# Performance work log

Measured on AMD Instinct MI355X. Metric: run time of the kernel, lower is better.

Reference implementation:

```python
import jax, jax.numpy as jnp
import numpy as np

B, S, D = 8, 1024, 768
H, DH = 8, 96          # number_of_heads, head_outdim = D // H
DFF = 4 * D            # mlp hidden
EPS = 1e-5


def _p(key, shape, scale=0.02):
    return (jax.random.normal(key, shape, dtype=jnp.float32) * scale)


def setup_inputs() -> dict:
    key = jax.random.key(0)
    ks = jax.random.split(key, 16)
    return {
        "h": jax.random.normal(ks[0], (B, S, D), dtype=jnp.float32),
        "x": jax.random.normal(ks[1], (B, S, D), dtype=jnp.float32),
        # SLN 1: scalar gamma/beta + LayerNorm affine
        "g1": jnp.ones((), jnp.float32), "be1": jnp.zeros((), jnp.float32),
        "ln1_w": jnp.ones((D,), jnp.float32), "ln1_b": jnp.zeros((D,), jnp.float32),
        # SLN 2
        "g2": jnp.ones((), jnp.float32), "be2": jnp.zeros((), jnp.float32),
        "ln2_w": jnp.ones((D,), jnp.float32), "ln2_b": jnp.zeros((D,), jnp.float32),
        # MSA projections (stored as [in, out] for x @ W)
        "Wq": _p(ks[2], (D, H * DH)), "bq": jnp.zeros((H * DH,), jnp.float32),
        "Wk": _p(ks[3], (D, H * DH)), "bk": jnp.zeros((H * DH,), jnp.float32),
        "Wv": _p(ks[4], (D, H * DH)), "bv": jnp.zeros((H * DH,), jnp.float32),
        "Wo": _p(ks[5], (H * DH, D)), "bo": jnp.zeros((D,), jnp.float32),
        # MLP: D -> 4D -> D, relu
        "W1": _p(ks[6], (D, DFF)), "b1": jnp.zeros((DFF,), jnp.float32),
        "W2": _p(ks[7], (DFF, D)), "b2": jnp.zeros((D,), jnp.float32),
    }


def _sln(h, x, gamma, beta, w, b):
    # SLN(h, x) = gamma * x * LayerNorm(h) + beta * x
    mu = jnp.mean(h, axis=-1, keepdims=True)
    var = jnp.var(h, axis=-1, keepdims=True)
    ln = (h - mu) * jax.lax.rsqrt(var + EPS) * w + b
    return gamma * x * ln + beta * x


def _l2_msa(h, Wq, bq, Wk, bk, Wv, bv, Wo, bo):
    # L2-distance multi-head self-attention (lp=2)
    def heads(W, bias):
        y = h @ W + bias                      # [B,S,H*DH]
        return y.reshape(B, S, H, DH).transpose(0, 2, 1, 3)  # [B,H,S,DH]
    q, k, v = heads(Wq, bq), heads(Wk, bk), heads(Wv, bv)
    # pairwise L2 distances via the quadratic expansion (avoids [B,H,S,S,DH])
    q2 = jnp.sum(q * q, axis=-1)              # [B,H,S]
    k2 = jnp.sum(k * k, axis=-1)              # [B,H,S]
    qk = jnp.einsum("bhsd,bhtd->bhst", q, k)  # [B,H,S,S]
    d2 = jnp.maximum(q2[..., :, None] + k2[..., None, :] - 2.0 * qk, 0.0)
    dist = jnp.sqrt(d2)                       # cdist(q, k, p=2)
    attn = jax.nn.softmax(-dist / np.sqrt(DH), axis=-1)
    out = jnp.einsum("bhst,bhtd->bhsd", attn, v)  # [B,H,S,DH]
    out = out.transpose(0, 2, 1, 3).reshape(B, S, H * DH)
    return out @ Wo + bo


def reference(h, x, g1, be1, ln1_w, ln1_b, g2, be2, ln2_w, ln2_b,
              Wq, bq, Wk, bk, Wv, bv, Wo, bo, W1, b1, W2, b2):
    h1 = _sln(h, x, g1, be1, ln1_w, ln1_b)
    htmp = _l2_msa(h1, Wq, bq, Wk, bk, Wv, bv, Wo, bo) + h   # dropout_rate=0 -> identity
    h2 = _sln(htmp, x, g2, be2, ln2_w, ln2_b)
    hf = jax.nn.relu(h2 @ W1 + b1) @ W2 + b2 + htmp
    return (x, hf)
```

## Files before the change

kernel.cpp:

```cpp
#include <hip/hip_runtime.h>
#include <math.h>

#define B_ 8
#define S_ 1024
#define D_ 768
#define H_ 8
#define DH_ 96
#define DFF_ 3072
#define NTOK (B_*S_)
#define QKVW 2304
#define EPS_ 1e-5f

typedef __attribute__((ext_vector_type(4))) float f4;
typedef __attribute__((ext_vector_type(4))) int i4;
typedef __attribute__((ext_vector_type(8))) __bf16 bf16x8;
typedef __attribute__((ext_vector_type(4))) unsigned short us4;
typedef __attribute__((ext_vector_type(8))) unsigned short us8;

static __device__ __forceinline__ unsigned short f2bf(float f) {
    unsigned int u = __builtin_bit_cast(unsigned int, f);
    u += 0x7fffu + ((u >> 16) & 1u);
    return (unsigned short)(u >> 16);
}
static __device__ __forceinline__ float bf2f(unsigned short u) {
    unsigned int x = ((unsigned int)u) << 16;
    return __builtin_bit_cast(float, x);
}

#define GLOBAL_LOAD_LDS16(g, l) \
    __builtin_amdgcn_global_load_lds((const __attribute__((address_space(1))) unsigned int*)(g), \
                                     (__attribute__((address_space(3))) unsigned int*)(l), 16, 0, 0)

__global__ __launch_bounds__(192) void sln_kernel(
    const float* __restrict__ h, const float* __restrict__ x,
    const float* __restrict__ gamma, const float* __restrict__ beta,
    const float* __restrict__ w, const float* __restrict__ bvec,
    unsigned short* __restrict__ out_bf, float* __restrict__ xcopy)
{
    int row = blockIdx.x;
    int t = threadIdx.x;
    const float4* h4 = (const float4*)(h + (size_t)row * D_);
    const float4* x4 = (const float4*)(x + (size_t)row * D_);
    float4 hv = h4[t];
    float s  = hv.x + hv.y + hv.z + hv.w;
    float ss = hv.x*hv.x + hv.y*hv.y + hv.z*hv.z + hv.w*hv.w;
    #pragma unroll
    for (int off = 32; off > 0; off >>= 1) {
        s  += __shfl_down(s, off);
        ss += __shfl_down(ss, off);
    }
    __shared__ float red[2][3];
    int wid = t >> 6;
    if ((t & 63) == 0) { red[0][wid] = s; red[1][wid] = ss; }
    __syncthreads();
    float sum   = red[0][0] + red[0][1] + red[0][2];
    float sumsq = red[1][0] + red[1][1] + red[1][2];
    float mu  = sum * (1.0f / D_);
    float var = sumsq * (1.0f / D_) - mu * mu;
    float rstd = rsqrtf(var + EPS_);
    float g = gamma[0], be = beta[0];
    float4 wv = ((const float4*)w)[t];
    float4 bv = ((const float4*)bvec)[t];
    float4 xv = x4[t];
    us4 o;
    o.x = f2bf(xv.x * (g * ((hv.x - mu) * rstd * wv.x + bv.x) + be));
    o.y = f2bf(xv.y * (g * ((hv.y - mu) * rstd * wv.y + bv.y) + be));
    o.z = f2bf(xv.z * (g * ((hv.z - mu) * rstd * wv.z + bv.z) + be));
    o.w = f2bf(xv.w * (g * ((hv.w - mu) * rstd * wv.w + bv.w) + be));
    *(us4*)(out_bf + (size_t)row * D_ + t * 4) = o;
    if (xcopy) ((float4*)(xcopy + (size_t)row * D_))[t] = xv;
}

__global__ __launch_bounds__(256) void transpose_bf16_kernel(
    const float* __restrict__ in, unsigned short* __restrict__ out, int K, int N)
{
    __shared__ float tile[32][33];
    int n0 = blockIdx.x * 32, k0 = blockIdx.y * 32;
    int tx = threadIdx.x, ty = threadIdx.y;
    #pragma unroll
    for (int r = 0; r < 4; r++)
        tile[ty + r * 8][tx] = in[(size_t)(k0 + ty + r * 8) * N + n0 + tx];
    __syncthreads();
    #pragma unroll
    for (int r = 0; r < 4; r++)
        out[(size_t)(n0 + ty + r * 8) * K + k0 + tx] = f2bf(tile[tx][ty + r * 8]);
}

__global__ void concat_bias_kernel(const float* __restrict__ bq, const float* __restrict__ bk,
                                   const float* __restrict__ bv, float* __restrict__ outb)
{
    int i = blockIdx.x * 256 + threadIdx.x;
    if (i >= QKVW) return;
    float v = (i < 768) ? bq[i] : (i < 1536) ? bk[i - 768] : bv[i - 1536];
    outb[i] = v;
}

template<int OUT_BF16, int RELU>
__global__ __launch_bounds__(256) void gemm_mfma_kernel(
    const unsigned short* __restrict__ A, const unsigned short* __restrict__ Bt,
    const float* __restrict__ bias, const float* __restrict__ resid,
    void* __restrict__ Cout, int M, int N, int K)
{
    __shared__ unsigned short Asm[128 * 32];
    __shared__ unsigned short Bsm[128 * 32];

    int t = threadIdx.x;
    int lane = t & 63, wv = t >> 6;
    int wm = wv & 1, wn = wv >> 1;
    int l16 = lane & 15, quad = lane >> 4;

    int bm = blockIdx.x * 128;
    int bn = blockIdx.y * 128;

    const unsigned short* Abase = A  + (size_t)bm * K;
    const unsigned short* Bbase = Bt + (size_t)bn * K;

    int fl0 = t, fl1 = 256 + t;
    int r0s = fl0 >> 2, kc0 = (fl0 & 3) << 3;
    int r1s = fl1 >> 2, kc1 = (fl1 & 3) << 3;

    f4 acc[4][4] = {};

    for (int k0 = 0; k0 < K; k0 += 32) {
        __syncthreads();
        GLOBAL_LOAD_LDS16(Abase + (size_t)r0s * K + k0 + kc0, &Asm[fl0 * 8]);
        GLOBAL_LOAD_LDS16(Abase + (size_t)r1s * K + k0 + kc1, &Asm[fl1 * 8]);
        GLOBAL_LOAD_LDS16(Bbase + (size_t)r0s * K + k0 + kc0, &Bsm[fl0 * 8]);
        GLOBAL_LOAD_LDS16(Bbase + (size_t)r1s * K + k0 + kc1, &Bsm[fl1 * 8]);
        __syncthreads();

        bf16x8 xf[4], wf[4];
        #pragma unroll
        for (int i = 0; i < 4; i++) {
            int m = wm * 64 + i * 16 + l16;
            xf[i] = __builtin_bit_cast(bf16x8, *(const i4*)&Asm[m * 32 + quad * 8]);
        }
        #pragma unroll
        for (int j = 0; j < 4; j++) {
            int n = wn * 64 + j * 16 + l16;
            wf[j] = __builtin_bit_cast(bf16x8, *(const i4*)&Bsm[n * 32 + quad * 8]);
        }
        #pragma unroll
        for (int j = 0; j < 4; j++)
            #pragma unroll
            for (int i = 0; i < 4; i++)
                acc[j][i] = __builtin_amdgcn_mfma_f32_16x16x32_bf16(wf[j], xf[i], acc[j][i], 0, 0, 0);
    }

    #pragma unroll
    for (int i = 0; i < 4; i++) {
        int rowg = bm + wm * 64 + i * 16 + l16;
        #pragma unroll
        for (int j = 0; j < 4; j++) {
            int colg0 = bn + wn * 64 + j * 16 + quad * 4;
            f4 v = acc[j][i];
            f4 b4 = *(const f4*)&bias[colg0];
            v += b4;
            if (RELU) {
                #pragma unroll
                for (int r = 0; r < 4; r++) v[r] = fmaxf(v[r], 0.f);
            }
            if (resid) {
                f4 r4 = *(const f4*)&resid[(size_t)rowg * N + colg0];
                v += r4;
            }
            if (OUT_BF16) {
                us4 o;
                o.x = f2bf(v[0]); o.y = f2bf(v[1]); o.z = f2bf(v[2]); o.w = f2bf(v[3]);
                *(us4*)((unsigned short*)Cout + (size_t)rowg * N + colg0) = o;
            } else {
                *(f4*)((float*)Cout + (size_t)rowg * N + colg0) = v;
            }
        }
    }
}

__global__ __launch_bounds__(256) void norms_kernel(
    const unsigned short* __restrict__ qkv, float* __restrict__ q2g, float* __restrict__ k2g)
{
    int row = blockIdx.x;
    int t = threadIdx.x;
    int hh = t >> 5, l32 = t & 31;
    const unsigned short* base = qkv + (size_t)row * QKVW + hh * DH_ + l32 * 3;
    float qs = 0.f, ks = 0.f;
    #pragma unroll
    for (int e = 0; e < 3; e++) {
        float qv = bf2f(base[e]);
        float kv = bf2f(base[768 + e]);
        qs += qv * qv; ks += kv * kv;
    }
    #pragma unroll
    for (int off = 16; off > 0; off >>= 1) {
        qs += __shfl_xor(qs, off, 32);
        ks += __shfl_xor(ks, off, 32);
    }
    if (l32 == 0) {
        int b = row >> 10, s = row & 1023;
        int idx = (b * H_ + hh) * S_ + s;
        q2g[idx] = qs; k2g[idx] = ks;
    }
}

__global__ __launch_bounds__(256) void vtrans_kernel(
    const unsigned short* __restrict__ qkv, unsigned short* __restrict__ vt)
{
    __shared__ unsigned short Vl[64][100];
    int blk = blockIdx.x;
    int bh = blk >> 4, kt = blk & 15;
    int b = bh >> 3, hh = bh & 7;
    int t = threadIdx.x;
    int key = t >> 2, qc = t & 3;
    const unsigned short* src = qkv + ((size_t)(b * S_ + kt * 64 + key)) * QKVW + 1536 + hh * DH_;
    #pragma unroll
    for (int i = 0; i < 3; i++) {
        int chunk = qc + i * 4;
        us8 v = *(const us8*)(src + chunk * 8);
        #pragma unroll
        for (int e = 0; e < 8; e++) Vl[key][chunk * 8 + e] = v[e];
    }
    __syncthreads();
    unsigned short* dst = vt + (size_t)blk * 7168;
    #pragma unroll
    for (int r = 0; r < 3; r++) {
        int c = r * 256 + t;
        int vd = c >> 3, kc = c & 7;
        us8 o;
        #pragma unroll
        for (int j = 0; j < 8; j++) o[j] = Vl[kc * 8 + j][vd];
        *(us8*)(dst + vd * 72 + kc * 8) = o;
    }
}

__global__ __launch_bounds__(256, 2) void attn_mfma_kernel(
    const unsigned short* __restrict__ qkv,
    const unsigned short* __restrict__ vt,
    const float* __restrict__ q2g, const float* __restrict__ k2g,
    unsigned short* __restrict__ outb)
{
    __shared__ unsigned short Klds[64 * 96];
    __shared__ unsigned short Vlds[7168];
    __shared__ unsigned short Plds[4][32 * 72];

    int t = threadIdx.x;
    int lane = t & 63, w = t >> 6;
    int l16 = lane & 15, quad = lane >> 4;

    int bh = blockIdx.x >> 3;
    int qt = blockIdx.x & 7;
    int b = bh >> 3, hh = bh & 7;

    int qrow0 = qt * 128 + w * 32;

    const unsigned short* qb = qkv + ((size_t)(b * S_ + qrow0)) * QKVW + hh * DH_;
    bf16x8 qf[2][3];
    #pragma unroll
    for (int n = 0; n < 2; n++)
        #pragma unroll
        for (int d = 0; d < 3; d++)
            qf[n][d] = __builtin_bit_cast(bf16x8,
                *(const i4*)(qb + (size_t)(n * 16 + l16) * QKVW + d * 32 + quad * 8));

    float q2n[2];
    q2n[0] = q2g[bh * S_ + qrow0 + l16];
    q2n[1] = q2g[bh * S_ + qrow0 + 16 + l16];

    float mrun[2] = {-INFINITY, -INFINITY};
    float lrun[2] = {0.f, 0.f};
    f4 Oacc[2][6] = {};

    const float rs = 0.10206207261596575f;

    const unsigned short* kgb = qkv + ((size_t)(b * S_)) * QKVW + 768 + hh * DH_;
    const unsigned short* vgb0 = vt + (size_t)(bh * 16) * 7168;

    for (int it = 0; it < 16; it++) {
        __syncthreads();
        #pragma unroll
        for (int r = 0; r < 3; r++) {
            int c = r * 256 + t;
            int key = c / 12, dc = c % 12;
            GLOBAL_LOAD_LDS16(kgb + ((size_t)(it * 64 + key)) * QKVW + dc * 8, &Klds[c * 8]);
        }
        const unsigned short* vgb = vgb0 + (size_t)it * 7168;
        #pragma unroll
        for (int r = 0; r < 3; r++)
            GLOBAL_LOAD_LDS16(vgb + (r * 256 + t) * 8, &Vlds[(r * 256 + t) * 8]);
        if (t < 128)
            GLOBAL_LOAD_LDS16(vgb + (768 + t) * 8, &Vlds[(768 + t) * 8]);
        __syncthreads();

        f4 sf[4][2];
        #pragma unroll
        for (int kt2 = 0; kt2 < 4; kt2++) {
            bf16x8 kf[3];
            #pragma unroll
            for (int d = 0; d < 3; d++)
                kf[d] = __builtin_bit_cast(bf16x8,
                    *(const i4*)&Klds[(kt2 * 16 + l16) * 96 + d * 32 + quad * 8]);
            #pragma unroll
            for (int n = 0; n < 2; n++) {
                f4 a = {};
                #pragma unroll
                for (int d = 0; d < 3; d++)
                    a = __builtin_amdgcn_mfma_f32_16x16x32_bf16(kf[d], qf[n][d], a, 0, 0, 0);
                sf[kt2][n] = a;
            }
        }
        #pragma unroll
        for (int kt2 = 0; kt2 < 4; kt2++) {
            float4 k2f = *(const float4*)(k2g + bh * S_ + it * 64 + kt2 * 16 + quad * 4);
            float k2a[4] = {k2f.x, k2f.y, k2f.z, k2f.w};
            #pragma unroll
            for (int n = 0; n < 2; n++) {
                f4 s = sf[kt2][n];
                #pragma unroll
                for (int r2 = 0; r2 < 4; r2++) {
                    float d2 = fmaxf(q2n[n] + k2a[r2] - 2.f * s[r2], 0.f);
                    s[r2] = -sqrtf(d2) * rs;
                }
                sf[kt2][n] = s;
            }
        }
        float alph[2];
        #pragma unroll
        for (int n = 0; n < 2; n++) {
            f4 m4 = sf[0][n];
            #pragma unroll
            for (int kt2 = 1; kt2 < 4; kt2++)
                #pragma unroll
                for (int r2 = 0; r2 < 4; r2++)
                    m4[r2] = fmaxf(m4[r2], sf[kt2][n][r2]);
            float mx = fmaxf(fmaxf(m4[0], m4[1]), fmaxf(m4[2], m4[3]));
            mx = fmaxf(mx, __shfl_xor(mx, 16, 64));
            mx = fmaxf(mx, __shfl_xor(mx, 32, 64));
            float mnew = fmaxf(mrun[n], mx);
            alph[n] = __expf(mrun[n] - mnew);
            mrun[n] = mnew;
            float ssum = 0.f;
            #pragma unroll
            for (int kt2 = 0; kt2 < 4; kt2++) {
                f4 s = sf[kt2][n];
                #pragma unroll
                for (int r2 = 0; r2 < 4; r2++) { s[r2] = __expf(s[r2] - mnew); ssum += s[r2]; }
                sf[kt2][n] = s;
            }
            ssum += __shfl_xor(ssum, 16, 64);
            ssum += __shfl_xor(ssum, 32, 64);
            lrun[n] = lrun[n] * alph[n] + ssum;
            #pragma unroll
            for (int kt2 = 0; kt2 < 4; kt2++) {
                f4 s = sf[kt2][n];
                uint2 pk;
                pk.x = (unsigned)f2bf(s[0]) | ((unsigned)f2bf(s[1]) << 16);
                pk.y = (unsigned)f2bf(s[2]) | ((unsigned)f2bf(s[3]) << 16);
                *(uint2*)&Plds[w][(n * 16 + l16) * 72 + kt2 * 16 + quad * 4] = pk;
            }
        }
        f4 av0, av1;
        #pragma unroll
        for (int r2 = 0; r2 < 4; r2++) {
            int src = quad * 4 + r2;
            av0[r2] = __shfl(alph[0], src, 64);
            av1[r2] = __shfl(alph[1], src, 64);
        }
        #pragma unroll
        for (int vtl = 0; vtl < 6; vtl++)
            #pragma unroll
            for (int r2 = 0; r2 < 4; r2++) {
                Oacc[0][vtl][r2] *= av0[r2];
                Oacc[1][vtl][r2] *= av1[r2];
            }
        bf16x8 pa[2][2];
        #pragma unroll
        for (int mt = 0; mt < 2; mt++)
            #pragma unroll
            for (int kf2 = 0; kf2 < 2; kf2++)
                pa[mt][kf2] = __builtin_bit_cast(bf16x8,
                    *(const i4*)&Plds[w][(mt * 16 + l16) * 72 + kf2 * 32 + quad * 8]);
        #pragma unroll
        for (int vtl = 0; vtl < 6; vtl++) {
            bf16x8 vf0 = __builtin_bit_cast(bf16x8,
                *(const i4*)&Vlds[(vtl * 16 + l16) * 72 + quad * 8]);
            bf16x8 vf1 = __builtin_bit_cast(bf16x8,
                *(const i4*)&Vlds[(vtl * 16 + l16) * 72 + 32 + quad * 8]);
            #pragma unroll
            for (int mt = 0; mt < 2; mt++) {
                Oacc[mt][vtl] = __builtin_amdgcn_mfma_f32_16x16x32_bf16(pa[mt][0], vf0, Oacc[mt][vtl], 0, 0, 0);
                Oacc[mt][vtl] = __builtin_amdgcn_mfma_f32_16x16x32_bf16(pa[mt][1], vf1, Oacc[mt][vtl], 0, 0, 0);
            }
        }
    }
    float inv0 = 1.f / lrun[0], inv1 = 1.f / lrun[1];
    f4 iv0, iv1;
    #pragma unroll
    for (int r2 = 0; r2 < 4; r2++) {
        int src = quad * 4 + r2;
        iv0[r2] = __shfl(inv0, src, 64);
        iv1[r2] = __shfl(inv1, src, 64);
    }
    #pragma unroll
    for (int mt = 0; mt < 2; mt++)
        #pragma unroll
        for (int vtl = 0; vtl < 6; vtl++)
            #pragma unroll
            for (int r2 = 0; r2 < 4; r2++) {
                int row = b * S_ + qrow0 + mt * 16 + quad * 4 + r2;
                float v = Oacc[mt][vtl][r2] * (mt == 0 ? iv0[r2] : iv1[r2]);
                outb[(size_t)row * D_ + hh * DH_ + vtl * 16 + l16] = f2bf(v);
            }
}

extern "C" void kernel_launch(void* const* d_in, const int* in_sizes, int n_in,
                              void* d_out, int out_size, void* d_ws, size_t ws_size,
                              hipStream_t stream)
{
    const float* h    = (const float*)d_in[0];
    const float* x    = (const float*)d_in[1];
    const float* g1   = (const float*)d_in[2];
    const float* be1  = (const float*)d_in[3];
    const float* ln1w = (const float*)d_in[4];
    const float* ln1b = (const float*)d_in[5];
    const float* g2   = (const float*)d_in[6];
    const float* be2  = (const float*)d_in[7];
    const float* ln2w = (const float*)d_in[8];
    const float* ln2b = (const float*)d_in[9];
    const float* Wq   = (const float*)d_in[10];
    const float* bq   = (const float*)d_in[11];
    const float* Wk   = (const float*)d_in[12];
    const float* bk   = (const float*)d_in[13];
    const float* Wv   = (const float*)d_in[14];
    const float* bv   = (const float*)d_in[15];
    const float* Wo   = (const float*)d_in[16];
    const float* bo   = (const float*)d_in[17];
    const float* W1   = (const float*)d_in[18];
    const float* b1   = (const float*)d_in[19];
    const float* W2   = (const float*)d_in[20];
    const float* b2   = (const float*)d_in[21];

    float* out = (float*)d_out;
    char* wsb = (char*)d_ws;
    const size_t ND = (size_t)NTOK * D_;

    size_t off = 0;
    unsigned short* W1t = (unsigned short*)(wsb + off); off += 4718592;
    unsigned short* W2t = (unsigned short*)(wsb + off); off += 4718592;
    float* bqkv = (float*)(wsb + off);                  off += 16384;
    float* htmp = (float*)(wsb + off);                  off += ND * 4;
    float* q2g  = (float*)(wsb + off);                  off += (size_t)B_ * H_ * S_ * 4;
    float* k2g  = (float*)(wsb + off);                  off += (size_t)B_ * H_ * S_ * 4;
    unsigned short* h2b = (unsigned short*)(wsb + off); off += ND * 2;
    size_t pool0 = off;
    unsigned short* Wqkvt = (unsigned short*)(wsb + off); off += 3538944;
    unsigned short* Wot   = (unsigned short*)(wsb + off); off += 1179648;
    unsigned short* h1b   = (unsigned short*)(wsb + off); off += ND * 2;
    unsigned short* vtg   = (unsigned short*)(wsb + off); off += (size_t)1024 * 14336;
    unsigned short* qkvb  = (unsigned short*)(wsb + off); off += (size_t)NTOK * QKVW * 2;
    unsigned short* attnb   = h1b;
    unsigned short* hiddenb = (unsigned short*)(wsb + pool0);

    dim3 tb(32, 8);
    transpose_bf16_kernel<<<dim3(768/32, 768/32), tb, 0, stream>>>(Wq, Wqkvt,              768, 768);
    transpose_bf16_kernel<<<dim3(768/32, 768/32), tb, 0, stream>>>(Wk, Wqkvt + 768*768,    768, 768);
    transpose_bf16_kernel<<<dim3(768/32, 768/32), tb, 0, stream>>>(Wv, Wqkvt + 2*768*768,  768, 768);
    transpose_bf16_kernel<<<dim3(768/32, 768/32), tb, 0, stream>>>(Wo, Wot, 768, 768);
    transpose_bf16_kernel<<<dim3(3072/32, 768/32), tb, 0, stream>>>(W1, W1t, 768, 3072);
    transpose_bf16_kernel<<<dim3(768/32, 3072/32), tb, 0, stream>>>(W2, W2t, 3072, 768);
    concat_bias_kernel<<<9, 256, 0, stream>>>(bq, bk, bv, bqkv);

    sln_kernel<<<NTOK, 192, 0, stream>>>(h, x, g1, be1, ln1w, ln1b, h1b, out);

    gemm_mfma_kernel<1, 0><<<dim3(NTOK/128, QKVW/128), 256, 0, stream>>>(
        h1b, Wqkvt, bqkv, nullptr, qkvb, NTOK, QKVW, D_);

    norms_kernel<<<NTOK, 256, 0, stream>>>(qkvb, q2g, k2g);
    vtrans_kernel<<<1024, 256, 0, stream>>>(qkvb, vtg);

    attn_mfma_kernel<<<512, 256, 0, stream>>>(qkvb, vtg, q2g, k2g, attnb);

    gemm_mfma_kernel<0, 0><<<dim3(NTOK/128, D_/128), 256, 0, stream>>>(
        attnb, Wot, bo, h, htmp, NTOK, D_, D_);

    sln_kernel<<<NTOK, 192, 0, stream>>>(htmp, x, g2, be2, ln2w, ln2b, h2b, nullptr);

    gemm_mfma_kernel<1, 1><<<dim3(NTOK/128, DFF_/128), 256, 0, stream>>>(
        h2b, W1t, b1, nullptr, hiddenb, NTOK, DFF_, D_);
    gemm_mfma_kernel<0, 0><<<dim3(NTOK/128, D_/128), 256, 0, stream>>>(
        hiddenb, W2t, b2, htmp, out + ND, NTOK, D_, DFF_);

    (void)in_sizes; (void)n_in; (void)out_size; (void)ws_size;
}
```

Baseline: 501.3 us.

## Halve attention query tile per wave and add 128x64 GEMM for N=768 outputs

The attention kernel now processes 16 query rows per wave instead of 32, doubling the grid to 1024 blocks. It raises the launch-bounds occupancy hint to 4 and switches softmax to exp2 with a folded scale constant. A new 128x64-tile GEMM kernel is used for the two projections with N=768, doubling their block count to improve CU fill. The trade-off is that each K/V tile loaded into LDS is reused by fewer query rows, so global and LDS traffic per useful FLOP rises.

Measured after the change: 468.7 us. 1.07x faster.

```diff
diff --git a/kernel.cpp b/kernel.cpp
--- a/kernel.cpp
+++ b/kernel.cpp
@@ -175,6 +175,85 @@
     }
 }
 
+template<int OUT_BF16, int RELU>
+__global__ __launch_bounds__(256) void gemm_mfma_n64_kernel(
+    const unsigned short* __restrict__ A, const unsigned short* __restrict__ Bt,
+    const float* __restrict__ bias, const float* __restrict__ resid,
+    void* __restrict__ Cout, int M, int N, int K)
+{
+    __shared__ unsigned short Asm[128 * 32];
+    __shared__ unsigned short Bsm[64 * 32];
+
+    int t = threadIdx.x;
+    int lane = t & 63, wv = t >> 6;
+    int wm = wv & 1, wn = wv >> 1;
+    int l16 = lane & 15, quad = lane >> 4;
+
+    int bm = blockIdx.x * 128;
+    int bn = blockIdx.y * 64;
+
+    const unsigned short* Abase = A  + (size_t)bm * K;
+    const unsigned short* Bbase = Bt + (size_t)bn * K;
+
+    int fl0 = t, fl1 = 256 + t;
+    int r0s = fl0 >> 2, kc0 = (fl0 & 3) << 3;
+    int r1s = fl1 >> 2, kc1 = (fl1 & 3) << 3;
+
+    f4 acc[2][4] = {};
+
+    for (int k0 = 0; k0 < K; k0 += 32) {
+        __syncthreads();
+        GLOBAL_LOAD_LDS16(Abase + (size_t)r0s * K + k0 + kc0, &Asm[fl0 * 8]);
+        GLOBAL_LOAD_LDS16(Abase + (size_t)r1s * K + k0 + kc1, &Asm[fl1 * 8]);
+        GLOBAL_LOAD_LDS16(Bbase + (size_t)r0s * K + k0 + kc0, &Bsm[fl0 * 8]);
+        __syncthreads();
+
+        bf16x8 xf[4], wf[2];
+        #pragma unroll
+        for (int i = 0; i < 4; i++) {
+            int m = wm * 64 + i * 16 + l16;
+            xf[i] = __builtin_bit_cast(bf16x8, *(const i4*)&Asm[m * 32 + quad * 8]);
+        }
+        #pragma unroll
+        for (int j = 0; j < 2; j++) {
+            int n = wn * 32 + j * 16 + l16;
+            wf[j] = __builtin_bit_cast(bf16x8, *(const i4*)&Bsm[n * 32 + quad * 8]);
+        }
+        #pragma unroll
+        for (int j = 0; j < 2; j++)
+            #pragma unroll
+            for (int i = 0; i < 4; i++)
+                acc[j][i] = __builtin_amdgcn_mfma_f32_16x16x32_bf16(wf[j], xf[i], acc[j][i], 0, 0, 0);
+    }
+
+    #pragma unroll
+    for (int i = 0; i < 4; i++) {
+        int rowg = bm + wm * 64 + i * 16 + l16;
+        #pragma unroll
+        for (int j = 0; j < 2; j++) {
+            int colg0 = bn + wn * 32 + j * 16 + quad * 4;
+            f4 v = acc[j][i];
+            f4 b4 = *(const f4*)&bias[colg0];
+            v += b4;
+            if (RELU) {
+                #pragma unroll
+                for (int r = 0; r < 4; r++) v[r] = fmaxf(v[r], 0.f);
+            }
+            if (resid) {
+                f4 r4 = *(const f4*)&resid[(size_t)rowg * N + colg0];
+                v += r4;
+            }
+            if (OUT_BF16) {
+                us4 o;
+                o.x = f2bf(v[0]); o.y = f2bf(v[1]); o.z = f2bf(v[2]); o.w = f2bf(v[3]);
+                *(us4*)((unsigned short*)Cout + (size_t)rowg * N + colg0) = o;
+            } else {
+                *(f4*)((float*)Cout + (size_t)rowg * N + colg0) = v;
+            }
+        }
+    }
+}
+
 __global__ __launch_bounds__(256) void norms_kernel(
     const unsigned short* __restrict__ qkv, float* __restrict__ q2g, float* __restrict__ k2g)
 {
@@ -231,7 +310,7 @@
     }
 }
 
-__global__ __launch_bounds__(256, 2) void attn_mfma_kernel(
+__global__ __launch_bounds__(256, 4) void attn_mfma_kernel(
     const unsigned short* __restrict__ qkv,
     const unsigned short* __restrict__ vt,
     const float* __restrict__ q2g, const float* __restrict__ k2g,
@@ -239,36 +318,32 @@
 {
     __shared__ unsigned short Klds[64 * 96];
     __shared__ unsigned short Vlds[7168];
-    __shared__ unsigned short Plds[4][32 * 72];
+    __shared__ unsigned short Plds[4][16 * 72];
 
     int t = threadIdx.x;
     int lane = t & 63, w = t >> 6;
     int l16 = lane & 15, quad = lane >> 4;
 
-    int bh = blockIdx.x >> 3;
-    int qt = blockIdx.x & 7;
+    int bh = blockIdx.x >> 4;
+    int qt = blockIdx.x & 15;
     int b = bh >> 3, hh = bh & 7;
 
-    int qrow0 = qt * 128 + w * 32;
+    int qrow0 = qt * 64 + w * 16;
 
     const unsigned short* qb = qkv + ((size_t)(b * S_ + qrow0)) * QKVW + hh * DH_;
-    bf16x8 qf[2][3];
-    #pragma unroll
-    for (int n = 0; n < 2; n++)
-        #pragma unroll
-        for (int d = 0; d < 3; d++)
-            qf[n][d] = __builtin_bit_cast(bf16x8,
-                *(const i4*)(qb + (size_t)(n * 16 + l16) * QKVW + d * 32 + quad * 8));
-
-    float q2n[2];
-    q2n[0] = q2g[bh * S_ + qrow0 + l16];
-    q2n[1] = q2g[bh * S_ + qrow0 + 16 + l16];
-
-    float mrun[2] = {-INFINITY, -INFINITY};
-    float lrun[2] = {0.f, 0.f};
-    f4 Oacc[2][6] = {};
-
-    const float rs = 0.10206207261596575f;
+    bf16x8 qf[3];
+    #pragma unroll
+    for (int d = 0; d < 3; d++)
+        qf[d] = __builtin_bit_cast(bf16x8,
+            *(const i4*)(qb + (size_t)l16 * QKVW + d * 32 + quad * 8));
+
+    float q2n = q2g[bh * S_ + qrow0 + l16];
+
+    float mrun = -INFINITY;
+    float lrun = 0.f;
+    f4 Oacc[6] = {};
+
+    const float cexp = 0.14724445f;
 
     const unsigned short* kgb = qkv + ((size_t)(b * S_)) * QKVW + 768 + hh * DH_;
     const unsigned short* vgb0 = vt + (size_t)(bh * 16) * 7168;
@@ -289,125 +364,92 @@
             GLOBAL_LOAD_LDS16(vgb + (768 + t) * 8, &Vlds[(768 + t) * 8]);
         __syncthreads();
 
-        f4 sf[4][2];
+        f4 sf[4];
         #pragma unroll
         for (int kt2 = 0; kt2 < 4; kt2++) {
-            bf16x8 kf[3];
-            #pragma unroll
-            for (int d = 0; d < 3; d++)
-                kf[d] = __builtin_bit_cast(bf16x8,
-                    *(const i4*)&Klds[(kt2 * 16 + l16) * 96 + d * 32 + quad * 8]);
-            #pragma unroll
-            for (int n = 0; n < 2; n++) {
-                f4 a = {};
-                #pragma unroll
-                for (int d = 0; d < 3; d++)
-                    a = __builtin_amdgcn_mfma_f32_16x16x32_bf16(kf[d], qf[n][d], a, 0, 0, 0);
-                sf[kt2][n] = a;
-            }
+            bf16x8 kf0 = __builtin_bit_cast(bf16x8, *(const i4*)&Klds[(kt2 * 16 + l16) * 96 + quad * 8]);
+            bf16x8 kf1 = __builtin_bit_cast(bf16x8, *(const i4*)&Klds[(kt2 * 16 + l16) * 96 + 32 + quad * 8]);
+            bf16x8 kf2 = __builtin_bit_cast(bf16x8, *(const i4*)&Klds[(kt2 * 16 + l16) * 96 + 64 + quad * 8]);
+            f4 a = {};
+            a = __builtin_amdgcn_mfma_f32_16x16x32_bf16(kf0, qf[0], a, 0, 0, 0);
+            a = __builtin_amdgcn_mfma_f32_16x16x32_bf16(kf1, qf[1], a, 0, 0, 0);
+            a = __builtin_amdgcn_mfma_f32_16x16x32_bf16(kf2, qf[2], a, 0, 0, 0);
+            sf[kt2] = a;
         }
         #pragma unroll
         for (int kt2 = 0; kt2 < 4; kt2++) {
             float4 k2f = *(const float4*)(k2g + bh * S_ + it * 64 + kt2 * 16 + quad * 4);
             float k2a[4] = {k2f.x, k2f.y, k2f.z, k2f.w};
+            f4 s = sf[kt2];
             #pragma unroll
-            for (int n = 0; n < 2; n++) {
-                f4 s = sf[kt2][n];
-                #pragma unroll
-                for (int r2 = 0; r2 < 4; r2++) {
-                    float d2 = fmaxf(q2n[n] + k2a[r2] - 2.f * s[r2], 0.f);
-                    s[r2] = -sqrtf(d2) * rs;
-                }
-                sf[kt2][n] = s;
-            }
-        }
-        float alph[2];
-        #pragma unroll
-        for (int n = 0; n < 2; n++) {
-            f4 m4 = sf[0][n];
+            for (int r2 = 0; r2 < 4; r2++) {
+                float d2 = fmaxf(q2n + k2a[r2] - 2.f * s[r2], 0.f);
+                s[r2] = -__builtin_amdgcn_sqrtf(d2) * cexp;
+            }
+            sf[kt2] = s;
+        }
+        f4 m4 = sf[0];
+        #pragma unroll
+        for (int kt2 = 1; kt2 < 4; kt2++)
             #pragma unroll
-            for (int kt2 = 1; kt2 < 4; kt2++)
-                #pragma unroll
-                for (int r2 = 0; r2 < 4; r2++)
-                    m4[r2] = fmaxf(m4[r2], sf[kt2][n][r2]);
-            float mx = fmaxf(fmaxf(m4[0], m4[1]), fmaxf(m4[2], m4[3]));
-            mx = fmaxf(mx, __shfl_xor(mx, 16, 64));
-            mx = fmaxf(mx, __shfl_xor(mx, 32, 64));
-            float mnew = fmaxf(mrun[n], mx);
-            alph[n] = __expf(mrun[n] - mnew);
-            mrun[n] = mnew;
-            float ssum = 0.f;
+            for (int r2 = 0; r2 < 4; r2++)
+                m4[r2] = fmaxf(m4[r2], sf[kt2][r2]);
+        float mx = fmaxf(fmaxf(m4[0], m4[1]), fmaxf(m4[2], m4[3]));
+        mx = fmaxf(mx, __shfl_xor(mx, 16, 64));
+        mx = fmaxf(mx, __shfl_xor(mx, 32, 64));
+        float mnew = fmaxf(mrun, mx);
+        float alph = exp2f(mrun - mnew);
+        mrun = mnew;
+        float ssum = 0.f;
+        #pragma unroll
+        for (int kt2 = 0; kt2 < 4; kt2++) {
+            f4 s = sf[kt2];
             #pragma unroll
-            for (int kt2 = 0; kt2 < 4; kt2++) {
-                f4 s = sf[kt2][n];
-                #pragma unroll
-                for (int r2 = 0; r2 < 4; r2++) { s[r2] = __expf(s[r2] - mnew); ssum += s[r2]; }
-                sf[kt2][n] = s;
-            }
-            ssum += __shfl_xor(ssum, 16, 64);
-            ssum += __shfl_xor(ssum, 32, 64);
-            lrun[n] = lrun[n] * alph[n] + ssum;
-            #pragma unroll
-            for (int kt2 = 0; kt2 < 4; kt2++) {
-                f4 s = sf[kt2][n];
-                uint2 pk;
-                pk.x = (unsigned)f2bf(s[0]) | ((unsigned)f2bf(s[1]) << 16);
-                pk.y = (unsigned)f2bf(s[2]) | ((unsigned)f2bf(s[3]) << 16);
-                *(uint2*)&Plds[w][(n * 16 + l16) * 72 + kt2 * 16 + quad * 4] = pk;
-            }
-        }
-        f4 av0, av1;
-        #pragma unroll
-        for (int r2 = 0; r2 < 4; r2++) {
-            int src = quad * 4 + r2;
-            av0[r2] = __shfl(alph[0], src, 64);
-            av1[r2] = __shfl(alph[1], src, 64);
-        }
+            for (int r2 = 0; r2 < 4; r2++) { s[r2] = exp2f(s[r2] - mnew); ssum += s[r2]; }
+            sf[kt2] = s;
+        }
+        ssum += __shfl_xor(ssum, 16, 64);
+        ssum += __shfl_xor(ssum, 32, 64);
+        lrun = lrun * alph + ssum;
+        #pragma unroll
+        for (int kt2 = 0; kt2 < 4; kt2++) {
+            f4 s = sf[kt2];
+            uint2 pk;
+            pk.x = (unsigned)f2bf(s[0]) | ((unsigned)f2bf(s[1]) << 16);
+            pk.y = (unsigned)f2bf(s[2]) | ((unsigned)f2bf(s[3]) << 16);
+            *(uint2*)&Plds[w][l16 * 72 + kt2 * 16 + quad * 4] = pk;
+        }
+        f4 av;
+        #pragma unroll
+        for (int r2 = 0; r2 < 4; r2++)
+            av[r2] = __shfl(alph, quad * 4 + r2, 64);
         #pragma unroll
         for (int vtl = 0; vtl < 6; vtl++)
             #pragma unroll
-            for (int r2 = 0; r2 < 4; r2++) {
-                Oacc[0][vtl][r2] *= av0[r2];
-                Oacc[1][vtl][r2] *= av1[r2];
-            }
-        bf16x8 pa[2][2];
-        #pragma unroll
-        for (int mt = 0; mt < 2; mt++)
-            #pragma unroll
-            for (int kf2 = 0; kf2 < 2; kf2++)
-                pa[mt][kf2] = __builtin_bit_cast(bf16x8,
-                    *(const i4*)&Plds[w][(mt * 16 + l16) * 72 + kf2 * 32 + quad * 8]);
+            for (int r2 = 0; r2 < 4; r2++)
+                Oacc[vtl][r2] *= av[r2];
+        bf16x8 pa0 = __builtin_bit_cast(bf16x8, *(const i4*)&Plds[w][l16 * 72 + quad * 8]);
+        bf16x8 pa1 = __builtin_bit_cast(bf16x8, *(const i4*)&Plds[w][l16 * 72 + 32 + quad * 8]);
         #pragma unroll
         for (int vtl = 0; vtl < 6; vtl++) {
-            bf16x8 vf0 = __builtin_bit_cast(bf16x8,
-                *(const i4*)&Vlds[(vtl * 16 + l16) * 72 + quad * 8]);
-            bf16x8 vf1 = __builtin_bit_cast(bf16x8,
-                *(const i4*)&Vlds[(vtl * 16 + l16) * 72 + 32 + quad * 8]);
-            #pragma unroll
-            for (int mt = 0; mt < 2; mt++) {
-                Oacc[mt][vtl] = __builtin_amdgcn_mfma_f32_16x16x32_bf16(pa[mt][0], vf0, Oacc[mt][vtl], 0, 0, 0);
-                Oacc[mt][vtl] = __builtin_amdgcn_mfma_f32_16x16x32_bf16(pa[mt][1], vf1, Oacc[mt][vtl], 0, 0, 0);
-            }
-        }
-    }
-    float inv0 = 1.f / lrun[0], inv1 = 1.f / lrun[1];
-    f4 iv0, iv1;
-    #pragma unroll
-    for (int r2 = 0; r2 < 4; r2++) {
-        int src = quad * 4 + r2;
-        iv0[r2] = __shfl(inv0, src, 64);
-        iv1[r2] = __shfl(inv1, src, 64);
-    }
-    #pragma unroll
-    for (int mt = 0; mt < 2; mt++)
-        #pragma unroll
-        for (int vtl = 0; vtl < 6; vtl++)
-            #pragma unroll
-            for (int r2 = 0; r2 < 4; r2++) {
-                int row = b * S_ + qrow0 + mt * 16 + quad * 4 + r2;
-                float v = Oacc[mt][vtl][r2] * (mt == 0 ? iv0[r2] : iv1[r2]);
-                outb[(size_t)row * D_ + hh * DH_ + vtl * 16 + l16] = f2bf(v);
-            }
+            bf16x8 vf0 = __builtin_bit_cast(bf16x8, *(const i4*)&Vlds[(vtl * 16 + l16) * 72 + quad * 8]);
+            bf16x8 vf1 = __builtin_bit_cast(bf16x8, *(const i4*)&Vlds[(vtl * 16 + l16) * 72 + 32 + quad * 8]);
+            Oacc[vtl] = __builtin_amdgcn_mfma_f32_16x16x32_bf16(pa0, vf0, Oacc[vtl], 0, 0, 0);
+            Oacc[vtl] = __builtin_amdgcn_mfma_f32_16x16x32_bf16(pa1, vf1, Oacc[vtl], 0, 0, 0);
+        }
+    }
+    float inv_l = 1.f / lrun;
+    f4 iv;
+    #pragma unroll
+    for (int r2 = 0; r2 < 4; r2++)
+        iv[r2] = __shfl(inv_l, quad * 4 + r2, 64);
+    #pragma unroll
+    for (int vtl = 0; vtl < 6; vtl++)
+        #pragma unroll
+        for (int r2 = 0; r2 < 4; r2++) {
+            int row = b * S_ + qrow0 + quad * 4 + r2;
+            outb[(size_t)row * D_ + hh * DH_ + vtl * 16 + l16] = f2bf(Oacc[vtl][r2] * iv[r2]);
+        }
 }
 
 extern "C" void kernel_launch(void* const* d_in, const int* in_sizes, int n_in,
@@ -475,16 +517,16 @@
     norms_kernel<<<NTOK, 256, 0, stream>>>(qkvb, q2g, k2g);
     vtrans_kernel<<<1024, 256, 0, stream>>>(qkvb, vtg);
 
-    attn_mfma_kernel<<<512, 256, 0, stream>>>(qkvb, vtg, q2g, k2g, attnb);
-
-    gemm_mfma_kernel<0, 0><<<dim3(NTOK/128, D_/128), 256, 0, stream>>>(
+    attn_mfma_kernel<<<1024, 256, 0, stream>>>(qkvb, vtg, q2g, k2g, attnb);
+
+    gemm_mfma_n64_kernel<0, 0><<<dim3(NTOK/128, D_/64), 256, 0, stream>>>(
         attnb, Wot, bo, h, htmp, NTOK, D_, D_);
 
     sln_kernel<<<NTOK, 192, 0, stream>>>(htmp, x, g2, be2, ln2w, ln2b, h2b, nullptr);
 
     gemm_mfma_kernel<1, 1><<<dim3(NTOK/128, DFF_/128), 256, 0, stream>>>(
         h2b, W1t, b1, nullptr, hiddenb, NTOK, DFF_, D_);
-    gemm_mfma_kernel<0, 0><<<dim3(NTOK/128, D_/128), 256, 0, stream>>>(
+    gemm_mfma_n64_kernel<0, 0><<<dim3(NTOK/128, D_/64), 256, 0, stream>>>(
         hiddenb, W2t, b2, htmp, out + ND, NTOK, D_, DFF_);
 
     (void)in_sizes; (void)n_in; (void)out_size; (void)ws_size;
```
